# Performance work log

Hardware: AMD Instinct MI355X
Metric: run time of the kernel (lower is better)

The kernel has to match this reference:

```python
import jax, jax.numpy as jnp
import numpy as np

B, S, HID = 1, 2048, 4096
NH, NKV, HD = 32, 8, 128
N_REP = NH // NKV
EPS = 1e-5
ROPE_THETA = 500000.0


def setup_inputs() -> dict:
    key = jax.random.key(0)
    ks = jax.random.split(key, 16)
    s = 0.02
    return {
        "hidden_states": jax.random.normal(ks[0], (B, S, HID), jnp.float32),
        "Wq": jax.random.normal(ks[1], (NH * HD, HID), jnp.float32) * s,
        "bq": jnp.zeros((NH * HD,), jnp.float32),
        "Wk": jax.random.normal(ks[2], (NKV * HD, HID), jnp.float32) * s,
        "bk": jnp.zeros((NKV * HD,), jnp.float32),
        "Wv": jax.random.normal(ks[3], (NKV * HD, HID), jnp.float32) * s,
        "bv": jnp.zeros((NKV * HD,), jnp.float32),
        "Wo": jax.random.normal(ks[4], (HID, HID), jnp.float32) * s,
        "bo": jnp.zeros((HID,), jnp.float32),
        "qn_g": jnp.ones((HD,), jnp.float32),
        "qn_b": jnp.zeros((HD,), jnp.float32),
        "kn_g": jnp.ones((HD,), jnp.float32),
        "kn_b": jnp.zeros((HD,), jnp.float32),
    }


def _layernorm(x, g, b):
    mu = jnp.mean(x, axis=-1, keepdims=True)
    var = jnp.var(x, axis=-1, keepdims=True)
    return (x - mu) * jax.lax.rsqrt(var + EPS) * g + b


def _rope_tables(seq_len, dtype):
    inv_freq = 1.0 / ROPE_THETA ** (jnp.arange(0, HD, 2, dtype=jnp.float32) / HD)
    pos = jnp.arange(seq_len, dtype=jnp.float32)
    freqs = pos[:, None] * inv_freq[None, :]          # (S, HD/2)
    emb = jnp.concatenate([freqs, freqs], axis=-1)    # (S, HD)
    return jnp.cos(emb).astype(dtype), jnp.sin(emb).astype(dtype)


def _rotate_half(x):
    x1, x2 = x[..., : HD // 2], x[..., HD // 2 :]
    return jnp.concatenate([-x2, x1], axis=-1)


def reference(hidden_states, Wq, bq, Wk, bk, Wv, bv, Wo, bo, qn_g, qn_b, kn_g, kn_b):
    x = hidden_states
    q = (x @ Wq.T + bq).reshape(B, S, NH, HD)
    k = (x @ Wk.T + bk).reshape(B, S, NKV, HD)
    v = (x @ Wv.T + bv).reshape(B, S, NKV, HD)
    # QK-Norm (LayerNorm over head_dim)
    q = _layernorm(q, qn_g, qn_b).transpose(0, 2, 1, 3)  # (B, NH, S, HD)
    k = _layernorm(k, kn_g, kn_b).transpose(0, 2, 1, 3)  # (B, NKV, S, HD)
    v = v.transpose(0, 2, 1, 3)
    # RoPE
    cos, sin = _rope_tables(S, x.dtype)  # (S, HD) each, broadcast over B, heads
    q = q * cos + _rotate_half(q) * sin
    k = k * cos + _rotate_half(k) * sin
    # GQA: repeat KV heads
    k = jnp.repeat(k, N_REP, axis=1)  # (B, NH, S, HD)
    v = jnp.repeat(v, N_REP, axis=1)
    # Causal attention
    scores = jnp.einsum("bhqd,bhkd->bhqk", q, k) / jnp.sqrt(jnp.float32(HD)).astype(x.dtype)
    causal = jnp.tril(jnp.ones((S, S), bool))
    scores = jnp.where(causal, scores, jnp.finfo(scores.dtype).min)
    attn = jax.nn.softmax(scores, axis=-1)
    out = jnp.einsum("bhqk,bhkd->bhqd", attn, v)
    out = out.transpose(0, 2, 1, 3).reshape(B, S, HID)
    return out @ Wo.T + bo
```

## Files before the change

kernel.cpp:

```cpp
#include <hip/hip_runtime.h>

typedef __bf16 bf16;
typedef __bf16 bf16x8 __attribute__((ext_vector_type(8)));
typedef __bf16 bf16x4 __attribute__((ext_vector_type(4)));
typedef float f32x4 __attribute__((ext_vector_type(4)));

#define S_LEN 2048
#define HID 4096
#define NH 32
#define NKV 8
#define HD 128
#define QSTR 6144
#define SCALE 0.08838834764831845f
#define QSCL 0.1275164918918885f
#define M2C 16.33f

template <int V> struct IC { static constexpr int value = V; };

__device__ __forceinline__ bf16x8 load8(const bf16* p) { return *(const bf16x8*)p; }
__device__ __forceinline__ bf16x8 load8(const float* p) {
    float4 a = *(const float4*)p;
    float4 b = *(const float4*)(p + 4);
    bf16x8 r;
    r[0] = (bf16)a.x; r[1] = (bf16)a.y; r[2] = (bf16)a.z; r[3] = (bf16)a.w;
    r[4] = (bf16)b.x; r[5] = (bf16)b.y; r[6] = (bf16)b.z; r[7] = (bf16)b.w;
    return r;
}

__device__ __forceinline__ void load_lds16(const bf16* g, bf16* l) {
    __builtin_amdgcn_global_load_lds(
        (const __attribute__((address_space(1))) void*)g,
        (__attribute__((address_space(3))) void*)l, 16, 0, 0);
}

template <int C> __device__ __forceinline__ void vmwait_if() {
    if constexpr (C >= 0) asm volatile("s_waitcnt vmcnt(%0)" ::"n"(C) : "memory");
}

__device__ __forceinline__ void lgkm0() {
    asm volatile("s_waitcnt lgkmcnt(0)" ::: "memory");
    __builtin_amdgcn_sched_barrier(0);
}

__global__ __launch_bounds__(256) void cvt(const float* __restrict__ in,
                                           bf16* __restrict__ out, int n8) {
    int i = blockIdx.x * 256 + threadIdx.x;
    if (i < n8) *(bf16x8*)&out[i * 8] = load8(&in[(size_t)i * 8]);
}

template <int BM, int BN, int WM, int WN, int BMODE, typename TO>
__global__ __launch_bounds__(512, 2) void gemm8(const bf16* __restrict__ A,
                                                const bf16* __restrict__ Bw,
                                                const float* __restrict__ b0,
                                                const float* __restrict__ b1,
                                                const float* __restrict__ b2,
                                                TO* __restrict__ out,
                                                int N, int K) {
    constexpr int RW  = BM / WM;
    constexpr int CW  = BN / WN;
    constexpr int FM  = RW / 16;
    constexpr int FN  = CW / 16;
    constexpr int FMH = FM / 2;
    constexpr int FNH0 = (FN + 1) / 2, FNH1 = FN - FNH0;
    constexpr int SZ0 = FNH0 * 16, SZ1 = FNH1 * 16;
    constexpr int AROWS_H = BM / 2;
    constexpr int B0ROWS = WN * SZ0, B1ROWS = WN * SZ1;
    constexpr int LA  = AROWS_H / 64;
    constexpr int LB0 = B0ROWS / 64, LB1 = B1ROWS / 64;
    constexpr int V0  = 2 * LA + LB0;
    constexpr int V3  = 2 * LA + LB0 + LB1;
    constexpr int V3T = LA + LB1;

    __shared__ __align__(16) bf16 AS[2 * BM * 64];
    __shared__ __align__(16) bf16 BS[2 * BN * 64];

    const int tid  = threadIdx.x;
    const int wave = tid >> 6;
    const int lane = tid & 63;
    const int quad = lane >> 4;
    const int l16  = lane & 15;
    const int wm   = wave / WN;
    const int wn   = wave % WN;

    const int gx   = gridDim.x;
    const int nwg  = gx * gridDim.y;
    const int orig = blockIdx.y * gx + blockIdx.x;
    int wg = orig;
    if ((nwg & 7) == 0) wg = (orig & 7) * (nwg >> 3) + (orig >> 3);
    const int row0 = (wg / gx) * BM;
    const int col0 = (wg % gx) * BN;

    auto stageA = [&](int mh, int bufv, int kt) {
#pragma unroll
        for (int j = 0; j < LA; ++j) {
            int c = j * 512 + tid;
            int r = c >> 3, pg = c & 7;
            int g = pg ^ (r & 7);
            int gr = (r / (RW / 2)) * RW + mh * (RW / 2) + (r % (RW / 2));
            load_lds16(&A[(size_t)(row0 + gr) * K + kt * 64 + g * 8],
                       &AS[bufv * (BM * 64) + mh * (AROWS_H * 64) + c * 8]);
        }
    };
    auto stageB0 = [&](int bufv, int kt) {
#pragma unroll
        for (int j = 0; j < LB0; ++j) {
            int c = j * 512 + tid;
            int r = c >> 3, pg = c & 7;
            int g = pg ^ (r & 7);
            int gc = (r / SZ0) * CW + (r % SZ0);
            load_lds16(&Bw[(size_t)(col0 + gc) * K + kt * 64 + g * 8],
                       &BS[bufv * (BN * 64) + c * 8]);
        }
    };
    auto stageB1 = [&](int bufv, int kt) {
#pragma unroll
        for (int j = 0; j < LB1; ++j) {
            int c = j * 512 + tid;
            int r = c >> 3, pg = c & 7;
            int g = pg ^ (r & 7);
            int gc = (r / SZ1) * CW + SZ0 + (r % SZ1);
            load_lds16(&Bw[(size_t)(col0 + gc) * K + kt * 64 + g * 8],
                       &BS[bufv * (BN * 64) + B0ROWS * 64 + c * 8]);
        }
    };

    f32x4 acc[FM][FN];
#pragma unroll
    for (int mi = 0; mi < FM; ++mi)
#pragma unroll
        for (int ni = 0; ni < FN; ++ni) { f32x4 z = {0.f, 0.f, 0.f, 0.f}; acc[mi][ni] = z; }

    bf16x8 af[FMH][2];
    bf16x8 bfv[FN][2];

    auto loadA = [&](int mh, int bufv) {
#pragma unroll
        for (int mi = 0; mi < FMH; ++mi)
#pragma unroll
            for (int ks = 0; ks < 2; ++ks) {
                int r = wm * (RW / 2) + mi * 16 + l16;
                int g = ks * 4 + quad;
                af[mi][ks] = *(const bf16x8*)&AS[bufv * (BM * 64) + mh * (AROWS_H * 64) +
                                                 r * 64 + ((g ^ (r & 7)) << 3)];
            }
    };
    auto loadB = [&](auto cNH, int bufv) {
        constexpr int NHv = decltype(cNH)::value;
        constexpr int CNT = NHv ? FNH1 : FNH0;
        constexpr int SZ  = NHv ? SZ1 : SZ0;
#pragma unroll
        for (int nj = 0; nj < CNT; ++nj)
#pragma unroll
            for (int ks = 0; ks < 2; ++ks) {
                int r = wn * SZ + nj * 16 + l16;
                int g = ks * 4 + quad;
                bfv[NHv * FNH0 + nj][ks] =
                    *(const bf16x8*)&BS[bufv * (BN * 64) + NHv * (B0ROWS * 64) +
                                        r * 64 + ((g ^ (r & 7)) << 3)];
            }
    };
    auto mmac = [&](auto cMH, auto cNH) {
        constexpr int MH = decltype(cMH)::value, NHv = decltype(cNH)::value;
        constexpr int NB = NHv ? FNH0 : 0, NE = NHv ? FN : FNH0;
        __builtin_amdgcn_s_setprio(1);
#pragma unroll
        for (int mi = 0; mi < FMH; ++mi)
#pragma unroll
            for (int ni = NB; ni < NE; ++ni)
#pragma unroll
                for (int ks = 0; ks < 2; ++ks)
                    acc[MH * FMH + mi][ni] = __builtin_amdgcn_mfma_f32_16x16x32_bf16(
                        af[mi][ks], bfv[ni][ks], acc[MH * FMH + mi][ni], 0, 0, 0);
        __builtin_amdgcn_s_setprio(0);
    };

    auto run_tile = [&](int t, auto cSA1, auto cSB1, auto cSA0, auto cSB0,
                        auto cV0, auto cV3) {
        const int buf = t & 1, nbuf = buf ^ 1;
        loadA(0, buf);
        loadB(IC<0>{}, buf);
        if constexpr (decltype(cSA1)::value) stageA(1, nbuf, t + 1);
        __builtin_amdgcn_s_barrier();
        lgkm0();
        mmac(IC<0>{}, IC<0>{});
        vmwait_if<decltype(cV0)::value>();
        __builtin_amdgcn_s_barrier();
        loadB(IC<1>{}, buf);
        if constexpr (decltype(cSB1)::value) stageB1(nbuf, t + 1);
        __builtin_amdgcn_s_barrier();
        lgkm0();
        mmac(IC<0>{}, IC<1>{});
        __builtin_amdgcn_s_barrier();
        loadA(1, buf);
        if constexpr (decltype(cSA0)::value) stageA(0, buf, t + 2);
        __builtin_amdgcn_s_barrier();
        lgkm0();
        mmac(IC<1>{}, IC<0>{});
        __builtin_amdgcn_s_barrier();
        if constexpr (decltype(cSB0)::value) stageB0(buf, t + 2);
        __builtin_amdgcn_s_barrier();
        lgkm0();
        mmac(IC<1>{}, IC<1>{});
        vmwait_if<decltype(cV3)::value>();
        __builtin_amdgcn_s_barrier();
    };

    stageA(0, 0, 0); stageB0(0, 0);
    stageA(1, 0, 0); stageB1(0, 0);
    stageA(0, 1, 1); stageB0(1, 1);
    vmwait_if<V3>();
    __builtin_amdgcn_s_barrier();

    const int NT = K >> 6;
    for (int t = 0; t < NT - 2; ++t)
        run_tile(t, IC<1>{}, IC<1>{}, IC<1>{}, IC<1>{}, IC<V0>{}, IC<V3>{});
    run_tile(NT - 2, IC<1>{}, IC<1>{}, IC<0>{}, IC<0>{}, IC<V0>{}, IC<V3T>{});
    run_tile(NT - 1, IC<0>{}, IC<0>{}, IC<0>{}, IC<0>{}, IC<0>{}, IC<-1>{});

#pragma unroll
    for (int ni = 0; ni < FN; ++ni) {
        int n = col0 + wn * CW + ni * 16 + l16;
        float bv;
        if (BMODE == 0) bv = b0[n];
        else bv = (n < 4096) ? b0[n] : ((n < 5120) ? b1[n - 4096] : b2[n - 5120]);
#pragma unroll
        for (int mi = 0; mi < FM; ++mi) {
            int m = row0 + wm * RW + mi * 16 + quad * 4;
#pragma unroll
            for (int reg = 0; reg < 4; ++reg)
                out[(size_t)(m + reg) * N + n] = (TO)(acc[mi][ni][reg] + bv);
        }
    }
}

__global__ __launch_bounds__(256) void ln_rope(bf16* __restrict__ qkv,
                                               const float* __restrict__ qg, const float* __restrict__ qbt,
                                               const float* __restrict__ kg, const float* __restrict__ kbt) {
    int row  = blockIdx.x * 4 + (threadIdx.x >> 6);
    int lane = threadIdx.x & 63;

    bf16* ptr;
    const float *g, *bb;
    int s;
    float osc;
    if (row < S_LEN * NH) {
        s   = row >> 5;
        ptr = qkv + (size_t)s * QSTR + (row & 31) * HD;
        g   = qg; bb = qbt; osc = QSCL;
    } else {
        int r2 = row - S_LEN * NH;
        s   = r2 >> 3;
        ptr = qkv + (size_t)s * QSTR + 4096 + (r2 & 7) * HD;
        g   = kg; bb = kbt; osc = 1.f;
    }

    float x1 = (float)ptr[lane];
    float x2 = (float)ptr[lane + 64];
    float sum = x1 + x2;
    float sq  = x1 * x1 + x2 * x2;
#pragma unroll
    for (int m = 1; m < 64; m <<= 1) {
        sum += __shfl_xor(sum, m);
        sq  += __shfl_xor(sq, m);
    }
    float mu  = sum * (1.f / 128.f);
    float var = sq * (1.f / 128.f) - mu * mu;
    float rs  = rsqrtf(var + 1e-5f);
    float n1  = (x1 - mu) * rs * g[lane] + bb[lane];
    float n2  = (x2 - mu) * rs * g[lane + 64] + bb[lane + 64];

    float inv = powf(500000.f, -(float)lane * (1.f / 64.f));
    float ang = (float)s * inv;
    float sn, cs;
    sincosf(ang, &sn, &cs);

    ptr[lane]      = (bf16)((n1 * cs - n2 * sn) * osc);
    ptr[lane + 64] = (bf16)((n2 * cs + n1 * sn) * osc);
}

__global__ __launch_bounds__(256) void transpose_v(const bf16* __restrict__ qkv,
                                                   bf16* __restrict__ vT) {
    __shared__ bf16 Ts[64 * 64];
    const int c0 = blockIdx.x * 64;
    const int s0 = blockIdx.y * 64;
    const int tid = threadIdx.x;

#pragma unroll
    for (int i = 0; i < 2; ++i) {
        int cc = i * 256 + tid;
        int r = cc >> 3, col8 = cc & 7;
        *(bf16x8*)&Ts[r * 64 + ((col8 ^ (r & 7)) << 3)] =
            *(const bf16x8*)&qkv[(size_t)(s0 + r) * QSTR + 5120 + c0 + (col8 << 3)];
    }
    __syncthreads();
#pragma unroll
    for (int i = 0; i < 2; ++i) {
        int oc = i * 256 + tid;
        int c = oc & 63, sb = oc >> 6;
        bf16x8 r8;
#pragma unroll
        for (int j = 0; j < 8; ++j) {
            int sg = sb * 8 + j;
            r8[j] = Ts[sg * 64 + ((((c >> 3) ^ (sg & 7)) << 3) + (c & 7))];
        }
        *(bf16x8*)&vT[(size_t)(c0 + c) * S_LEN + s0 + sb * 8] = r8;
    }
}

__global__ __launch_bounds__(256, 2) void attn3(const bf16* __restrict__ qkv,
                                                const bf16* __restrict__ vT,
                                                float* __restrict__ OP,
                                                float* __restrict__ lbuf) {
    const int pairp = blockIdx.x >> 1;
    const int sp    = blockIdx.x & 1;
    const int kvh   = blockIdx.y;
    const int tid   = threadIdx.x;
    const int wave  = tid >> 6;
    const int lane  = tid & 63;
    const int quad  = lane >> 4;
    const int l16   = lane & 15;
    const int h     = kvh * 4 + wave;

    __shared__ __align__(16) bf16 Ks[64 * 128];
    __shared__ __align__(16) bf16 Vt[128 * 64];
    __shared__ __align__(16) bf16 Ps[4][32 * 64];

    float* OPs = OP + (size_t)sp * (S_LEN * HID);
    float* lbs = lbuf + sp * (S_LEN * NH);

    bf16x8 onesf;
#pragma unroll
    for (int j = 0; j < 8; ++j) onesf[j] = (bf16)1.f;

    int4 pk[4], pv[4];

    for (int ph = 0; ph < 2; ++ph) {
        const int qt  = ph ? (63 - pairp) : pairp;
        const int r0  = qt * 32;
        const int nkt = qt / 2 + 1;
        const int nit = (nkt + 1 - sp) / 2;

        bf16x8 qf[2][4];
#pragma unroll
        for (int mi = 0; mi < 2; ++mi)
#pragma unroll
            for (int ks = 0; ks < 4; ++ks)
                qf[mi][ks] = *(const bf16x8*)&qkv[(size_t)(r0 + mi * 16 + l16) * QSTR +
                                                  h * HD + ks * 32 + quad * 8];

        f32x4 o_acc[2][8];
#pragma unroll
        for (int mi = 0; mi < 2; ++mi)
#pragma unroll
            for (int ni = 0; ni < 8; ++ni) {
                f32x4 z = {0.f, 0.f, 0.f, 0.f};
                o_acc[mi][ni] = z;
            }
        f32x4 lacc[2];
#pragma unroll
        for (int mi = 0; mi < 2; ++mi) { f32x4 z = {0.f, 0.f, 0.f, 0.f}; lacc[mi] = z; }

        auto load_regs = [&](int kt) {
#pragma unroll
            for (int i = 0; i < 4; ++i) {
                int cc = i * 256 + tid;
                int key = cc >> 4, d8 = cc & 15;
                pk[i] = *(const int4*)&qkv[(size_t)(kt * 64 + key) * QSTR + 4096 +
                                           kvh * HD + (d8 << 3)];
            }
#pragma unroll
            for (int i = 0; i < 4; ++i) {
                int cc = i * 256 + tid;
                int d = cc >> 3, k8 = cc & 7;
                pv[i] = *(const int4*)&vT[(size_t)(kvh * HD + d) * S_LEN + kt * 64 + (k8 << 3)];
            }
        };

        if (nit > 0) load_regs(sp);

        for (int it = 0; it < nit; ++it) {
            const int kt = sp + 2 * it;
#pragma unroll
            for (int i = 0; i < 4; ++i) {
                int cc = i * 256 + tid;
                int key = cc >> 4, d8 = cc & 15;
                *(int4*)&Ks[key * 128 + ((d8 ^ (key & 7)) << 3)] = pk[i];
            }
#pragma unroll
            for (int i = 0; i < 4; ++i) {
                int cc = i * 256 + tid;
                int d = cc >> 3, k8 = cc & 7;
                *(int4*)&Vt[d * 64 + ((k8 ^ (d & 7)) << 3)] = pv[i];
            }
            __syncthreads();

            if (it + 1 < nit) load_regs(kt + 2);

            f32x4 sacc[2][4];
#pragma unroll
            for (int mi = 0; mi < 2; ++mi)
#pragma unroll
                for (int ni = 0; ni < 4; ++ni) {
                    f32x4 z = {0.f, 0.f, 0.f, 0.f};
                    sacc[mi][ni] = z;
                }
#pragma unroll
            for (int ks = 0; ks < 4; ++ks)
#pragma unroll
                for (int ni = 0; ni < 4; ++ni) {
                    bf16x8 kf = *(const bf16x8*)&Ks[(ni * 16 + l16) * 128 +
                                                    ((((ks << 2) + quad) ^ (l16 & 7)) << 3)];
                    sacc[0][ni] = __builtin_amdgcn_mfma_f32_16x16x32_bf16(qf[0][ks], kf, sacc[0][ni], 0, 0, 0);
                    sacc[1][ni] = __builtin_amdgcn_mfma_f32_16x16x32_bf16(qf[1][ks], kf, sacc[1][ni], 0, 0, 0);
                }

#pragma unroll
            for (int mi = 0; mi < 2; ++mi)
#pragma unroll
                for (int reg = 0; reg < 4; ++reg) {
                    int rloc = mi * 16 + quad * 4 + reg;
                    int qrow = r0 + rloc;
#pragma unroll
                    for (int ni = 0; ni < 4; ++ni) {
                        int key = kt * 64 + ni * 16 + l16;
                        float t = (key > qrow) ? -1e30f : (sacc[mi][ni][reg] - M2C);
                        float p = exp2f(t);
                        int blk = (ni * 2 + (l16 >> 3)) ^ (rloc & 7);
                        Ps[wave][rloc * 64 + blk * 8 + (l16 & 7)] = (bf16)p;
                    }
                }

#pragma unroll
            for (int ks2 = 0; ks2 < 2; ++ks2) {
                bf16x8 pa[2];
#pragma unroll
                for (int mi = 0; mi < 2; ++mi) {
                    int rloc = mi * 16 + l16;
                    pa[mi] = *(const bf16x8*)&Ps[wave][rloc * 64 +
                                                       ((((ks2 << 2) + quad) ^ (rloc & 7)) << 3)];
                }
#pragma unroll
                for (int ni = 0; ni < 8; ++ni) {
                    int d = ni * 16 + l16;
                    bf16x8 vf = *(const bf16x8*)&Vt[d * 64 + ((((ks2 << 2) + quad) ^ (d & 7)) << 3)];
                    o_acc[0][ni] = __builtin_amdgcn_mfma_f32_16x16x32_bf16(pa[0], vf, o_acc[0][ni], 0, 0, 0);
                    o_acc[1][ni] = __builtin_amdgcn_mfma_f32_16x16x32_bf16(pa[1], vf, o_acc[1][ni], 0, 0, 0);
                }
                lacc[0] = __builtin_amdgcn_mfma_f32_16x16x32_bf16(pa[0], onesf, lacc[0], 0, 0, 0);
                lacc[1] = __builtin_amdgcn_mfma_f32_16x16x32_bf16(pa[1], onesf, lacc[1], 0, 0, 0);
            }
            __syncthreads();
        }

#pragma unroll
        for (int mi = 0; mi < 2; ++mi)
#pragma unroll
            for (int reg = 0; reg < 4; ++reg) {
                int s = r0 + mi * 16 + quad * 4 + reg;
#pragma unroll
                for (int ni = 0; ni < 8; ++ni)
                    OPs[(size_t)s * HID + h * HD + ni * 16 + l16] = o_acc[mi][ni][reg];
                if (l16 == 0) lbs[s * NH + h] = lacc[mi][reg];
            }
    }
}

__global__ __launch_bounds__(256) void merge(const float* __restrict__ OP,
                                             const float* __restrict__ lb,
                                             bf16* __restrict__ abuf) {
    int g = blockIdx.x * 256 + threadIdx.x;
    int s = g >> 10;
    int col = (g & 1023) << 2;
    int h = col >> 7;
    float l = lb[s * NH + h] + lb[S_LEN * NH + s * NH + h];
    float inv = 1.f / fmaxf(l, 1e-30f);
    f32x4 o0 = *(const f32x4*)&OP[(size_t)g << 2];
    f32x4 o1 = *(const f32x4*)&OP[((size_t)g << 2) + (size_t)S_LEN * HID];
    bf16x4 r;
#pragma unroll
    for (int j = 0; j < 4; ++j) r[j] = (bf16)((o0[j] + o1[j]) * inv);
    *(bf16x4*)&abuf[(size_t)s * HID + col] = r;
}

template <typename TA, typename TO>
__global__ __launch_bounds__(256) void gemm_bt(const TA* __restrict__ A,
                                               const float* __restrict__ W,
                                               const float* __restrict__ bias,
                                               TO* __restrict__ out,
                                               int N, int K) {
    __shared__ __align__(16) bf16 As[128 * 64];
    __shared__ __align__(16) bf16 Bs[128 * 64];
    const int tid = threadIdx.x, wave = tid >> 6, lane = tid & 63;
    const int quad = lane >> 4, l16 = lane & 15, wm = wave >> 1, wn = wave & 1;
    const int row0 = blockIdx.y * 128, col0 = blockIdx.x * 128;
    f32x4 acc[4][4];
#pragma unroll
    for (int mi = 0; mi < 4; ++mi)
#pragma unroll
        for (int ni = 0; ni < 4; ++ni) { f32x4 z = {0.f,0.f,0.f,0.f}; acc[mi][ni] = z; }
    for (int k0 = 0; k0 < K; k0 += 64) {
#pragma unroll
        for (int i = 0; i < 4; ++i) {
            int c = i * 256 + tid, r = c >> 3, col8 = (c & 7) << 3;
            *(bf16x8*)&As[r * 64 + col8] = load8(&A[(size_t)(row0 + r) * K + k0 + col8]);
            *(bf16x8*)&Bs[r * 64 + col8] = load8(&W[(size_t)(col0 + r) * K + k0 + col8]);
        }
        __syncthreads();
#pragma unroll
        for (int ks = 0; ks < 2; ++ks) {
            bf16x8 af[4], bfr[4];
#pragma unroll
            for (int mi = 0; mi < 4; ++mi)
                af[mi] = *(const bf16x8*)&As[(wm * 64 + mi * 16 + l16) * 64 + ks * 32 + quad * 8];
#pragma unroll
            for (int ni = 0; ni < 4; ++ni)
                bfr[ni] = *(const bf16x8*)&Bs[(wn * 64 + ni * 16 + l16) * 64 + ks * 32 + quad * 8];
#pragma unroll
            for (int mi = 0; mi < 4; ++mi)
#pragma unroll
                for (int ni = 0; ni < 4; ++ni)
                    acc[mi][ni] = __builtin_amdgcn_mfma_f32_16x16x32_bf16(af[mi], bfr[ni], acc[mi][ni], 0, 0, 0);
        }
        __syncthreads();
    }
#pragma unroll
    for (int ni = 0; ni < 4; ++ni) {
        int n = col0 + wn * 64 + ni * 16 + l16;
        float bv = bias[n];
#pragma unroll
        for (int mi = 0; mi < 4; ++mi) {
            int m = row0 + wm * 64 + mi * 16 + quad * 4;
#pragma unroll
            for (int reg = 0; reg < 4; ++reg)
                out[(size_t)(m + reg) * N + n] = (TO)(acc[mi][ni][reg] + bv);
        }
    }
}

__global__ __launch_bounds__(256) void ln_rope_f(bf16* __restrict__ qb, bf16* __restrict__ kb,
                                                 const float* __restrict__ qg, const float* __restrict__ qbt,
                                                 const float* __restrict__ kg, const float* __restrict__ kbt) {
    int row = blockIdx.x * 4 + (threadIdx.x >> 6);
    int lane = threadIdx.x & 63;
    bf16* ptr; const float *g, *bb; int s;
    if (row < S_LEN * NH) { s = row >> 5; ptr = qb + (size_t)s * (NH * HD) + (row & 31) * HD; g = qg; bb = qbt; }
    else { int r2 = row - S_LEN * NH; s = r2 >> 3; ptr = kb + (size_t)s * (NKV * HD) + (r2 & 7) * HD; g = kg; bb = kbt; }
    float x1 = (float)ptr[lane], x2 = (float)ptr[lane + 64];
    float sum = x1 + x2, sq = x1 * x1 + x2 * x2;
#pragma unroll
    for (int m = 1; m < 64; m <<= 1) { sum += __shfl_xor(sum, m); sq += __shfl_xor(sq, m); }
    float mu = sum * (1.f / 128.f), var = sq * (1.f / 128.f) - mu * mu;
    float rs = rsqrtf(var + 1e-5f);
    float n1 = (x1 - mu) * rs * g[lane] + bb[lane];
    float n2 = (x2 - mu) * rs * g[lane + 64] + bb[lane + 64];
    float inv = powf(500000.f, -(float)lane * (1.f / 64.f));
    float ang = (float)s * inv, sn, cs;
    sincosf(ang, &sn, &cs);
    ptr[lane] = (bf16)(n1 * cs - n2 * sn);
    ptr[lane + 64] = (bf16)(n2 * cs + n1 * sn);
}

__global__ __launch_bounds__(256) void attn_old(const bf16* __restrict__ qbuf,
                                                const bf16* __restrict__ kbuf,
                                                const bf16* __restrict__ vbuf,
                                                bf16* __restrict__ obuf) {
    const int qi = blockIdx.x, hh = blockIdx.y, kvh = hh >> 2;
    __shared__ __align__(16) bf16 Qs[64 * 128];
    __shared__ __align__(16) bf16 Ks2[64 * 128];
    __shared__ __align__(16) bf16 Vt2[128 * 80];
    __shared__ __align__(16) float Ss[64 * 64];
    __shared__ __align__(16) bf16 Ps2[64 * 64];
    __shared__ float mS[64], lS[64], aS[64];
    const int tid = threadIdx.x, wave = tid >> 6, lane = tid & 63;
    const int quad = lane >> 4, l16 = lane & 15;
#pragma unroll
    for (int i = 0; i < 4; ++i) {
        int c = i * 256 + tid, r = c >> 4, col8 = (c & 15) << 3;
        *(int4*)&Qs[r * 128 + col8] = *(const int4*)&qbuf[(size_t)(qi * 64 + r) * HID + hh * HD + col8];
    }
    if (tid < 64) { mS[tid] = -1e30f; lS[tid] = 0.f; }
    f32x4 o_acc[8];
#pragma unroll
    for (int i = 0; i < 8; ++i) { f32x4 z = {0.f,0.f,0.f,0.f}; o_acc[i] = z; }
    __syncthreads();
    for (int kt = 0; kt <= qi; ++kt) {
#pragma unroll
        for (int i = 0; i < 4; ++i) {
            int c = i * 256 + tid, r = c >> 4, col8 = (c & 15) << 3;
            const size_t gofs = (size_t)(kt * 64 + r) * (NKV * HD) + kvh * HD + col8;
            *(int4*)&Ks2[r * 128 + col8] = *(const int4*)&kbuf[gofs];
            bf16x8 vv = *(const bf16x8*)&vbuf[gofs];
#pragma unroll
            for (int e = 0; e < 8; ++e) Vt2[(col8 + e) * 80 + r] = vv[e];
        }
        __syncthreads();
        f32x4 sacc[4];
#pragma unroll
        for (int ni = 0; ni < 4; ++ni) { f32x4 z = {0.f,0.f,0.f,0.f}; sacc[ni] = z; }
#pragma unroll
        for (int ks = 0; ks < 4; ++ks) {
            bf16x8 a = *(const bf16x8*)&Qs[(wave * 16 + l16) * 128 + ks * 32 + quad * 8];
#pragma unroll
            for (int ni = 0; ni < 4; ++ni) {
                bf16x8 b = *(const bf16x8*)&Ks2[(ni * 16 + l16) * 128 + ks * 32 + quad * 8];
                sacc[ni] = __builtin_amdgcn_mfma_f32_16x16x32_bf16(a, b, sacc[ni], 0, 0, 0);
            }
        }
#pragma unroll
        for (int ni = 0; ni < 4; ++ni)
#pragma unroll
            for (int reg = 0; reg < 4; ++reg) {
                int r = wave * 16 + quad * 4 + reg, cc = ni * 16 + l16;
                float sv = sacc[ni][reg] * SCALE;
                if (kt * 64 + cc > qi * 64 + r) sv = -1e30f;
                Ss[r * 64 + cc] = sv;
            }
        __syncthreads();
        {
            int r = tid >> 2, j = tid & 3;
            float vals[16], mloc = -1e30f;
#pragma unroll
            for (int c = 0; c < 16; ++c) { vals[c] = Ss[r * 64 + j * 16 + c]; mloc = fmaxf(mloc, vals[c]); }
            mloc = fmaxf(mloc, __shfl_xor(mloc, 1));
            mloc = fmaxf(mloc, __shfl_xor(mloc, 2));
            float mold = mS[r], mnew = fmaxf(mold, mloc), ssum = 0.f;
#pragma unroll
            for (int c = 0; c < 16; ++c) {
                float p = __expf(vals[c] - mnew);
                ssum += p;
                Ps2[r * 64 + j * 16 + c] = (bf16)p;
            }
            ssum += __shfl_xor(ssum, 1);
            ssum += __shfl_xor(ssum, 2);
            if (j == 0) { float alpha = __expf(mold - mnew); mS[r] = mnew; lS[r] = lS[r] * alpha + ssum; aS[r] = alpha; }
        }
        __syncthreads();
        {
            float al2[4];
#pragma unroll
            for (int reg = 0; reg < 4; ++reg) al2[reg] = aS[wave * 16 + quad * 4 + reg];
#pragma unroll
            for (int ni = 0; ni < 8; ++ni)
#pragma unroll
                for (int reg = 0; reg < 4; ++reg) o_acc[ni][reg] *= al2[reg];
#pragma unroll
            for (int ks = 0; ks < 2; ++ks) {
                bf16x8 a = *(const bf16x8*)&Ps2[(wave * 16 + l16) * 64 + ks * 32 + quad * 8];
#pragma unroll
                for (int ni = 0; ni < 8; ++ni) {
                    bf16x8 b = *(const bf16x8*)&Vt2[(ni * 16 + l16) * 80 + ks * 32 + quad * 8];
                    o_acc[ni] = __builtin_amdgcn_mfma_f32_16x16x32_bf16(a, b, o_acc[ni], 0, 0, 0);
                }
            }
        }
        __syncthreads();
    }
    {
        float linv[4];
#pragma unroll
        for (int reg = 0; reg < 4; ++reg) linv[reg] = 1.f / fmaxf(lS[wave * 16 + quad * 4 + reg], 1e-20f);
#pragma unroll
        for (int ni = 0; ni < 8; ++ni)
#pragma unroll
            for (int reg = 0; reg < 4; ++reg) {
                int r = wave * 16 + quad * 4 + reg;
                obuf[(size_t)(qi * 64 + r) * HID + hh * HD + ni * 16 + l16] = (bf16)(o_acc[ni][reg] * linv[reg]);
            }
    }
}

extern "C" void kernel_launch(void* const* d_in, const int* in_sizes, int n_in,
                              void* d_out, int out_size, void* d_ws, size_t ws_size,
                              hipStream_t stream) {
    const float* x   = (const float*)d_in[0];
    const float* Wq  = (const float*)d_in[1];
    const float* bq  = (const float*)d_in[2];
    const float* Wk  = (const float*)d_in[3];
    const float* bk  = (const float*)d_in[4];
    const float* Wv  = (const float*)d_in[5];
    const float* bv  = (const float*)d_in[6];
    const float* Wo  = (const float*)d_in[7];
    const float* bo  = (const float*)d_in[8];
    const float* qg  = (const float*)d_in[9];
    const float* qbt = (const float*)d_in[10];
    const float* kg  = (const float*)d_in[11];
    const float* kbt = (const float*)d_in[12];
    float* out = (float*)d_out;

    const size_t NEED = 130547712;
    if (ws_size >= NEED) {
        char* p = (char*)d_ws;
        bf16*  xb   = (bf16*)p;
        bf16*  Wqkv = (bf16*)(p + 16777216);
        float* OP   = (float*)p;
        bf16*  Wob  = (bf16*)(p + 67108864);
        bf16*  qkv  = (bf16*)(p + 100663296);
        bf16*  abuf = (bf16*)(p + 100663296);
        bf16*  vT   = (bf16*)(p + 125829120);
        float* lbuf = (float*)(p + 130023424);

        cvt<<<4096, 256, 0, stream>>>(x,  xb, 1048576);
        cvt<<<8192, 256, 0, stream>>>(Wq, Wqkv, 2097152);
        cvt<<<2048, 256, 0, stream>>>(Wk, Wqkv + (size_t)4096 * 4096, 524288);
        cvt<<<2048, 256, 0, stream>>>(Wv, Wqkv + (size_t)5120 * 4096, 524288);
        cvt<<<8192, 256, 0, stream>>>(Wo, Wob, 2097152);

        gemm8<256, 192, 2, 4, 1, bf16><<<dim3(32, 8), 512, 0, stream>>>(
            xb, Wqkv, bq, bk, bv, qkv, QSTR, 4096);

        ln_rope<<<dim3((S_LEN * (NH + NKV)) / 4), 256, 0, stream>>>(qkv, qg, qbt, kg, kbt);

        transpose_v<<<dim3(16, 32), 256, 0, stream>>>(qkv, vT);

        attn3<<<dim3(64, 8), 256, 0, stream>>>(qkv, vT, OP, lbuf);
        merge<<<8192, 256, 0, stream>>>(OP, lbuf, abuf);

        gemm8<256, 128, 4, 2, 0, float><<<dim3(32, 8), 512, 0, stream>>>(
            abuf, Wob, bo, bo, bo, out, 4096, 4096);
    } else {
        char* ws = (char*)d_ws;
        bf16* qbuf = (bf16*)(ws);
        bf16* kbuf = (bf16*)(ws + (16u << 20));
        bf16* vbuf = (bf16*)(ws + (20u << 20));
        bf16* abuf = (bf16*)(ws + (24u << 20));
        gemm_bt<float, bf16><<<dim3(32, 16), 256, 0, stream>>>(x, Wq, bq, qbuf, 4096, 4096);
        gemm_bt<float, bf16><<<dim3(8, 16), 256, 0, stream>>>(x, Wk, bk, kbuf, 1024, 4096);
        gemm_bt<float, bf16><<<dim3(8, 16), 256, 0, stream>>>(x, Wv, bv, vbuf, 1024, 4096);
        ln_rope_f<<<dim3((S_LEN * (NH + NKV)) / 4), 256, 0, stream>>>(qbuf, kbuf, qg, qbt, kg, kbt);
        attn_old<<<dim3(32, 32), 256, 0, stream>>>(qbuf, kbuf, vbuf, abuf);
        gemm_bt<bf16, float><<<dim3(32, 16), 256, 0, stream>>>(abuf, Wo, bo, out, 4096, 4096);
    }
}
```

Measured before the change: 578.4 us.

## Merge split-KV attention halves in LDS and fuse the five conversion kernels

The attention kernel now runs both key-split halves in one 512-thread block, with eight waves across two KV tiles. It combines the partial outputs and row sums through shared memory and writes normalized bf16 directly. This removes the fp32 partial-output buffers and the separate merge kernel. The five fp32→bf16 conversion launches are folded into one kernel, and the RoPE frequency powf is replaced with exp2f. In exchange, attention now launches half as many blocks, uses much larger LDS per block, and adds extra block-wide barriers per phase.

```diff
diff --git a/kernel.cpp b/kernel.cpp
--- a/kernel.cpp
+++ b/kernel.cpp
@@ -42,10 +42,23 @@
     __builtin_amdgcn_sched_barrier(0);
 }
 
-__global__ __launch_bounds__(256) void cvt(const float* __restrict__ in,
-                                           bf16* __restrict__ out, int n8) {
+__global__ __launch_bounds__(256) void cvt5(const float* __restrict__ x,
+                                            const float* __restrict__ Wq,
+                                            const float* __restrict__ Wk,
+                                            const float* __restrict__ Wv,
+                                            const float* __restrict__ Wo,
+                                            bf16* __restrict__ xb,
+                                            bf16* __restrict__ Wqkv,
+                                            bf16* __restrict__ Wob) {
     int i = blockIdx.x * 256 + threadIdx.x;
-    if (i < n8) *(bf16x8*)&out[i * 8] = load8(&in[(size_t)i * 8]);
+    const float* src;
+    bf16* dst;
+    if (i < 1048576)      { src = x  + (size_t)i * 8;              dst = xb + (size_t)i * 8; }
+    else if (i < 3145728) { size_t j = i - 1048576; src = Wq + j * 8; dst = Wqkv + j * 8; }
+    else if (i < 3670016) { size_t j = i - 3145728; src = Wk + j * 8; dst = Wqkv + 16777216 + j * 8; }
+    else if (i < 4194304) { size_t j = i - 3670016; src = Wv + j * 8; dst = Wqkv + 20971520 + j * 8; }
+    else                  { size_t j = i - 4194304; src = Wo + j * 8; dst = Wob + j * 8; }
+    *(bf16x8*)dst = load8(src);
 }
 
 template <int BM, int BN, int WM, int WN, int BMODE, typename TO>
@@ -269,7 +282,7 @@
     float n1  = (x1 - mu) * rs * g[lane] + bb[lane];
     float n2  = (x2 - mu) * rs * g[lane + 64] + bb[lane + 64];
 
-    float inv = powf(500000.f, -(float)lane * (1.f / 64.f));
+    float inv = exp2f(-0.2958057514f * (float)lane);
     float ang = (float)s * inv;
     float sn, cs;
     sincosf(ang, &sn, &cs);
@@ -307,26 +320,25 @@
     }
 }
 
-__global__ __launch_bounds__(256, 2) void attn3(const bf16* __restrict__ qkv,
-                                                const bf16* __restrict__ vT,
-                                                float* __restrict__ OP,
-                                                float* __restrict__ lbuf) {
-    const int pairp = blockIdx.x >> 1;
-    const int sp    = blockIdx.x & 1;
+__global__ __launch_bounds__(512) void attn4(const bf16* __restrict__ qkv,
+                                             const bf16* __restrict__ vT,
+                                             bf16* __restrict__ abuf) {
+    const int pairp = blockIdx.x;
     const int kvh   = blockIdx.y;
     const int tid   = threadIdx.x;
     const int wave  = tid >> 6;
     const int lane  = tid & 63;
     const int quad  = lane >> 4;
     const int l16   = lane & 15;
-    const int h     = kvh * 4 + wave;
-
-    __shared__ __align__(16) bf16 Ks[64 * 128];
-    __shared__ __align__(16) bf16 Vt[128 * 64];
-    __shared__ __align__(16) bf16 Ps[4][32 * 64];
-
-    float* OPs = OP + (size_t)sp * (S_LEN * HID);
-    float* lbs = lbuf + sp * (S_LEN * NH);
+    const int spw   = wave >> 2;
+    const int hw    = wave & 3;
+    const int h     = kvh * 4 + hw;
+
+    __shared__ __align__(16) bf16 smem[2 * 64 * 128 + 2 * 128 * 64 + 8 * 32 * 64];
+    __shared__ float Ls[8][32];
+    bf16* Ksb = smem;
+    bf16* Vtb = smem + 2 * 64 * 128;
+    bf16* Psb = smem + 2 * 64 * 128 + 2 * 128 * 64;
 
     bf16x8 onesf;
 #pragma unroll
@@ -338,7 +350,7 @@
         const int qt  = ph ? (63 - pairp) : pairp;
         const int r0  = qt * 32;
         const int nkt = qt / 2 + 1;
-        const int nit = (nkt + 1 - sp) / 2;
+        const int nit = (nkt + 1) >> 1;
 
         bf16x8 qf[2][4];
 #pragma unroll
@@ -360,126 +372,148 @@
 #pragma unroll
         for (int mi = 0; mi < 2; ++mi) { f32x4 z = {0.f, 0.f, 0.f, 0.f}; lacc[mi] = z; }
 
-        auto load_regs = [&](int kt) {
+        auto load_regs = [&](int kt0) {
 #pragma unroll
             for (int i = 0; i < 4; ++i) {
-                int cc = i * 256 + tid;
-                int key = cc >> 4, d8 = cc & 15;
-                pk[i] = *(const int4*)&qkv[(size_t)(kt * 64 + key) * QSTR + 4096 +
+                int cc = i * 512 + tid;
+                int tile = cc >> 10, g = cc & 1023;
+                int key = g >> 4, d8 = g & 15;
+                pk[i] = *(const int4*)&qkv[(size_t)((kt0 + tile) * 64 + key) * QSTR + 4096 +
                                            kvh * HD + (d8 << 3)];
             }
 #pragma unroll
             for (int i = 0; i < 4; ++i) {
-                int cc = i * 256 + tid;
-                int d = cc >> 3, k8 = cc & 7;
-                pv[i] = *(const int4*)&vT[(size_t)(kvh * HD + d) * S_LEN + kt * 64 + (k8 << 3)];
+                int cc = i * 512 + tid;
+                int tile = cc >> 10, g = cc & 1023;
+                int d = g >> 3, k8 = g & 7;
+                pv[i] = *(const int4*)&vT[(size_t)(kvh * HD + d) * S_LEN +
+                                          (kt0 + tile) * 64 + (k8 << 3)];
             }
         };
 
-        if (nit > 0) load_regs(sp);
+        load_regs(0);
 
         for (int it = 0; it < nit; ++it) {
-            const int kt = sp + 2 * it;
 #pragma unroll
             for (int i = 0; i < 4; ++i) {
-                int cc = i * 256 + tid;
-                int key = cc >> 4, d8 = cc & 15;
-                *(int4*)&Ks[key * 128 + ((d8 ^ (key & 7)) << 3)] = pk[i];
+                int cc = i * 512 + tid;
+                int tile = cc >> 10, g = cc & 1023;
+                int key = g >> 4, d8 = g & 15;
+                *(int4*)&Ksb[tile * 8192 + key * 128 + ((d8 ^ (key & 7)) << 3)] = pk[i];
             }
 #pragma unroll
             for (int i = 0; i < 4; ++i) {
-                int cc = i * 256 + tid;
-                int d = cc >> 3, k8 = cc & 7;
-                *(int4*)&Vt[d * 64 + ((k8 ^ (d & 7)) << 3)] = pv[i];
+                int cc = i * 512 + tid;
+                int tile = cc >> 10, g = cc & 1023;
+                int d = g >> 3, k8 = g & 7;
+                *(int4*)&Vtb[tile * 8192 + d * 64 + ((k8 ^ (d & 7)) << 3)] = pv[i];
             }
             __syncthreads();
 
-            if (it + 1 < nit) load_regs(kt + 2);
-
-            f32x4 sacc[2][4];
+            if (it + 1 < nit) load_regs(2 * (it + 1));
+
+            const int kt = 2 * it + spw;
+            if (kt < nkt) {
+                const bf16* Kw = Ksb + spw * 8192;
+                const bf16* Vw = Vtb + spw * 8192;
+                bf16* Pw = Psb + wave * 2048;
+
+                f32x4 sacc[2][4];
+#pragma unroll
+                for (int mi = 0; mi < 2; ++mi)
+#pragma unroll
+                    for (int ni = 0; ni < 4; ++ni) {
+                        f32x4 z = {0.f, 0.f, 0.f, 0.f};
+                        sacc[mi][ni] = z;
+                    }
+#pragma unroll
+                for (int ks = 0; ks < 4; ++ks)
+#pragma unroll
+                    for (int ni = 0; ni < 4; ++ni) {
+                        bf16x8 kf = *(const bf16x8*)&Kw[(ni * 16 + l16) * 128 +
+                                                        ((((ks << 2) + quad) ^ (l16 & 7)) << 3)];
+                        sacc[0][ni] = __builtin_amdgcn_mfma_f32_16x16x32_bf16(qf[0][ks], kf, sacc[0][ni], 0, 0, 0);
+                        sacc[1][ni] = __builtin_amdgcn_mfma_f32_16x16x32_bf16(qf[1][ks], kf, sacc[1][ni], 0, 0, 0);
+                    }
+
+#pragma unroll
+                for (int mi = 0; mi < 2; ++mi)
+#pragma unroll
+                    for (int reg = 0; reg < 4; ++reg) {
+                        int rloc = mi * 16 + quad * 4 + reg;
+                        int qrow = r0 + rloc;
+#pragma unroll
+                        for (int ni = 0; ni < 4; ++ni) {
+                            int key = kt * 64 + ni * 16 + l16;
+                            float t = (key > qrow) ? -1e30f : (sacc[mi][ni][reg] - M2C);
+                            float p = exp2f(t);
+                            int blk = (ni * 2 + (l16 >> 3)) ^ (rloc & 7);
+                            Pw[rloc * 64 + blk * 8 + (l16 & 7)] = (bf16)p;
+                        }
+                    }
+
+#pragma unroll
+                for (int ks2 = 0; ks2 < 2; ++ks2) {
+                    bf16x8 pa[2];
+#pragma unroll
+                    for (int mi = 0; mi < 2; ++mi) {
+                        int rloc = mi * 16 + l16;
+                        pa[mi] = *(const bf16x8*)&Pw[rloc * 64 +
+                                                     ((((ks2 << 2) + quad) ^ (rloc & 7)) << 3)];
+                    }
+#pragma unroll
+                    for (int ni = 0; ni < 8; ++ni) {
+                        int d = ni * 16 + l16;
+                        bf16x8 vf = *(const bf16x8*)&Vw[d * 64 + ((((ks2 << 2) + quad) ^ (d & 7)) << 3)];
+                        o_acc[0][ni] = __builtin_amdgcn_mfma_f32_16x16x32_bf16(pa[0], vf, o_acc[0][ni], 0, 0, 0);
+                        o_acc[1][ni] = __builtin_amdgcn_mfma_f32_16x16x32_bf16(pa[1], vf, o_acc[1][ni], 0, 0, 0);
+                    }
+                    lacc[0] = __builtin_amdgcn_mfma_f32_16x16x32_bf16(pa[0], onesf, lacc[0], 0, 0, 0);
+                    lacc[1] = __builtin_amdgcn_mfma_f32_16x16x32_bf16(pa[1], onesf, lacc[1], 0, 0, 0);
+                }
+            }
+            __syncthreads();
+        }
+
+        float* M = (float*)smem;
+        if (spw == 1) {
+            float* Mw = M + hw * 4096;
 #pragma unroll
             for (int mi = 0; mi < 2; ++mi)
 #pragma unroll
-                for (int ni = 0; ni < 4; ++ni) {
-                    f32x4 z = {0.f, 0.f, 0.f, 0.f};
-                    sacc[mi][ni] = z;
-                }
-#pragma unroll
-            for (int ks = 0; ks < 4; ++ks)
-#pragma unroll
-                for (int ni = 0; ni < 4; ++ni) {
-                    bf16x8 kf = *(const bf16x8*)&Ks[(ni * 16 + l16) * 128 +
-                                                    ((((ks << 2) + quad) ^ (l16 & 7)) << 3)];
-                    sacc[0][ni] = __builtin_amdgcn_mfma_f32_16x16x32_bf16(qf[0][ks], kf, sacc[0][ni], 0, 0, 0);
-                    sacc[1][ni] = __builtin_amdgcn_mfma_f32_16x16x32_bf16(qf[1][ks], kf, sacc[1][ni], 0, 0, 0);
-                }
-
-#pragma unroll
-            for (int mi = 0; mi < 2; ++mi)
-#pragma unroll
-                for (int reg = 0; reg < 4; ++reg) {
-                    int rloc = mi * 16 + quad * 4 + reg;
-                    int qrow = r0 + rloc;
-#pragma unroll
-                    for (int ni = 0; ni < 4; ++ni) {
-                        int key = kt * 64 + ni * 16 + l16;
-                        float t = (key > qrow) ? -1e30f : (sacc[mi][ni][reg] - M2C);
-                        float p = exp2f(t);
-                        int blk = (ni * 2 + (l16 >> 3)) ^ (rloc & 7);
-                        Ps[wave][rloc * 64 + blk * 8 + (l16 & 7)] = (bf16)p;
+                for (int ni = 0; ni < 8; ++ni)
+#pragma unroll
+                    for (int j = 0; j < 4; ++j)
+                        Mw[((mi * 8 + ni) * 4 + j) * 64 + lane] = o_acc[mi][ni][j];
+            if (l16 == 0)
+#pragma unroll
+                for (int mi = 0; mi < 2; ++mi)
+#pragma unroll
+                    for (int reg = 0; reg < 4; ++reg)
+                        Ls[wave][mi * 16 + quad * 4 + reg] = lacc[mi][reg];
+        }
+        __syncthreads();
+        if (spw == 0) {
+            float* Mw = M + hw * 4096;
+#pragma unroll
+            for (int mi = 0; mi < 2; ++mi) {
+                float linv[4];
+#pragma unroll
+                for (int reg = 0; reg < 4; ++reg)
+                    linv[reg] = 1.f / fmaxf(lacc[mi][reg] +
+                                            Ls[wave + 4][mi * 16 + quad * 4 + reg], 1e-30f);
+#pragma unroll
+                for (int ni = 0; ni < 8; ++ni)
+#pragma unroll
+                    for (int reg = 0; reg < 4; ++reg) {
+                        float v = o_acc[mi][ni][reg] + Mw[((mi * 8 + ni) * 4 + reg) * 64 + lane];
+                        int s = r0 + mi * 16 + quad * 4 + reg;
+                        abuf[(size_t)s * HID + h * HD + ni * 16 + l16] = (bf16)(v * linv[reg]);
                     }
-                }
-
-#pragma unroll
-            for (int ks2 = 0; ks2 < 2; ++ks2) {
-                bf16x8 pa[2];
-#pragma unroll
-                for (int mi = 0; mi < 2; ++mi) {
-                    int rloc = mi * 16 + l16;
-                    pa[mi] = *(const bf16x8*)&Ps[wave][rloc * 64 +
-                                                       ((((ks2 << 2) + quad) ^ (rloc & 7)) << 3)];
-                }
-#pragma unroll
-                for (int ni = 0; ni < 8; ++ni) {
-                    int d = ni * 16 + l16;
-                    bf16x8 vf = *(const bf16x8*)&Vt[d * 64 + ((((ks2 << 2) + quad) ^ (d & 7)) << 3)];
-                    o_acc[0][ni] = __builtin_amdgcn_mfma_f32_16x16x32_bf16(pa[0], vf, o_acc[0][ni], 0, 0, 0);
-                    o_acc[1][ni] = __builtin_amdgcn_mfma_f32_16x16x32_bf16(pa[1], vf, o_acc[1][ni], 0, 0, 0);
-                }
-                lacc[0] = __builtin_amdgcn_mfma_f32_16x16x32_bf16(pa[0], onesf, lacc[0], 0, 0, 0);
-                lacc[1] = __builtin_amdgcn_mfma_f32_16x16x32_bf16(pa[1], onesf, lacc[1], 0, 0, 0);
-            }
-            __syncthreads();
-        }
-
-#pragma unroll
-        for (int mi = 0; mi < 2; ++mi)
-#pragma unroll
-            for (int reg = 0; reg < 4; ++reg) {
-                int s = r0 + mi * 16 + quad * 4 + reg;
-#pragma unroll
-                for (int ni = 0; ni < 8; ++ni)
-                    OPs[(size_t)s * HID + h * HD + ni * 16 + l16] = o_acc[mi][ni][reg];
-                if (l16 == 0) lbs[s * NH + h] = lacc[mi][reg];
-            }
-    }
-}
-
-__global__ __launch_bounds__(256) void merge(const float* __restrict__ OP,
-                                             const float* __restrict__ lb,
-                                             bf16* __restrict__ abuf) {
-    int g = blockIdx.x * 256 + threadIdx.x;
-    int s = g >> 10;
-    int col = (g & 1023) << 2;
-    int h = col >> 7;
-    float l = lb[s * NH + h] + lb[S_LEN * NH + s * NH + h];
-    float inv = 1.f / fmaxf(l, 1e-30f);
-    f32x4 o0 = *(const f32x4*)&OP[(size_t)g << 2];
-    f32x4 o1 = *(const f32x4*)&OP[((size_t)g << 2) + (size_t)S_LEN * HID];
-    bf16x4 r;
-#pragma unroll
-    for (int j = 0; j < 4; ++j) r[j] = (bf16)((o0[j] + o1[j]) * inv);
-    *(bf16x4*)&abuf[(size_t)s * HID + col] = r;
+            }
+        }
+        __syncthreads();
+    }
 }
 
 template <typename TA, typename TO>
@@ -692,18 +726,12 @@
         char* p = (char*)d_ws;
         bf16*  xb   = (bf16*)p;
         bf16*  Wqkv = (bf16*)(p + 16777216);
-        float* OP   = (float*)p;
+        bf16*  abuf = (bf16*)p;
         bf16*  Wob  = (bf16*)(p + 67108864);
         bf16*  qkv  = (bf16*)(p + 100663296);
-        bf16*  abuf = (bf16*)(p + 100663296);
         bf16*  vT   = (bf16*)(p + 125829120);
-        float* lbuf = (float*)(p + 130023424);
-
-        cvt<<<4096, 256, 0, stream>>>(x,  xb, 1048576);
-        cvt<<<8192, 256, 0, stream>>>(Wq, Wqkv, 2097152);
-        cvt<<<2048, 256, 0, stream>>>(Wk, Wqkv + (size_t)4096 * 4096, 524288);
-        cvt<<<2048, 256, 0, stream>>>(Wv, Wqkv + (size_t)5120 * 4096, 524288);
-        cvt<<<8192, 256, 0, stream>>>(Wo, Wob, 2097152);
+
+        cvt5<<<24576, 256, 0, stream>>>(x, Wq, Wk, Wv, Wo, xb, Wqkv, Wob);
 
         gemm8<256, 192, 2, 4, 1, bf16><<<dim3(32, 8), 512, 0, stream>>>(
             xb, Wqkv, bq, bk, bv, qkv, QSTR, 4096);
@@ -712,8 +740,7 @@
 
         transpose_v<<<dim3(16, 32), 256, 0, stream>>>(qkv, vT);
 
-        attn3<<<dim3(64, 8), 256, 0, stream>>>(qkv, vT, OP, lbuf);
-        merge<<<8192, 256, 0, stream>>>(OP, lbuf, abuf);
+        attn4<<<dim3(32, 8), 512, 0, stream>>>(qkv, vT, abuf);
 
         gemm8<256, 128, 4, 2, 0, float><<<dim3(32, 8), 512, 0, stream>>>(
             abuf, Wob, bo, bo, bo, out, 4096, 4096);
```

New measurement: 556.8 us. 3.7% less time.
